# Performance work log

Hardware: AMD Instinct MI355X
Metric: run time of the kernel (lower is better)

## Reference

```python
import jax, jax.numpy as jnp
import numpy as np
from jax import lax

B, A, T, D, V, K = 16, 1024, 512, 256, 50000, 3
EXP_DILS = [1, 2, 4, 8, 16, 32, 32]  # conv_num=7, exp_num=5
REF_DILS = [1, 1, 1]                 # refine_num=3


def setup_inputs() -> dict:
    key = jax.random.key(0)
    ks = jax.random.split(key, 14)
    inp = {
        'article_word': jax.random.randint(ks[0], (B, A), 0, V),
        'article_char': jax.random.randint(ks[1], (B, A, 16), 0, 100),
        'template_word': jax.random.randint(ks[2], (B, T), 0, V),
        'template_char': jax.random.randint(ks[3], (B, T, 16), 0, 100),
        'article_mask': jnp.ones((B, A), jnp.float32),
        'template_mask': jnp.ones((B, T), jnp.float32),
        'emb': jax.random.normal(ks[4], (V, D), jnp.float32) * 0.02,
        'exp_w': jax.random.normal(ks[5], (7, K, D, 2 * D), jnp.float32) * 0.03,
        'exp_b': jnp.zeros((7, 2 * D), jnp.float32),
        'ref_w': jax.random.normal(ks[6], (3, K, D, 2 * D), jnp.float32) * 0.03,
        'ref_b': jnp.zeros((3, 2 * D), jnp.float32),
        'ff1_w': jax.random.normal(ks[7], (10, 10), jnp.float32) * 0.3,
        'ff1_b': jnp.zeros((10,), jnp.float32),
        'ff2_w': jax.random.normal(ks[8], (10, 1), jnp.float32) * 0.3,
        'ff2_b': jnp.zeros((1,), jnp.float32),
    }
    return inp


def _res_block(x, w, b, dilation):
    # x: [B, L, D]; w: [K, D, 2D]  (Conv1d, padding='same' given k//2*dilation)
    pad = (K // 2) * dilation
    y = lax.conv_general_dilated(x, w, window_strides=(1,), padding=[(pad, pad)],
                                 rhs_dilation=(dilation,),
                                 dimension_numbers=('NWC', 'WIO', 'NWC')) + b
    a, g = jnp.split(y, 2, axis=2)  # GLU on channel dim
    return x + a * jax.nn.sigmoid(g)


def _encode(x, exp_w, exp_b, ref_w, ref_b):
    for i, d in enumerate(EXP_DILS):
        x = _res_block(x, exp_w[i], exp_b[i], d)
    for i, d in enumerate(REF_DILS):
        x = _res_block(x, ref_w[i], ref_b[i], d)
    return x  # dropout is identity in eval mode


def reference(article_word, article_char, template_word, template_char,
              article_mask, template_mask, emb, exp_w, exp_b, ref_w, ref_b,
              ff1_w, ff1_b, ff2_w, ff2_b):
    art = _encode(emb[article_word], exp_w, exp_b, ref_w, ref_b)    # [B,A,D]
    tpl = _encode(emb[template_word], exp_w, exp_b, ref_w, ref_b)   # [B,T,D]
    # pairwise squared distance without materializing [B,A,T,D]
    a2 = jnp.sum(art * art, axis=-1)                 # [B,A]
    t2 = jnp.sum(tpl * tpl, axis=-1)                 # [B,T]
    dot = jnp.einsum('bad,btd->bat', art, tpl)       # [B,A,T]
    dist = jnp.maximum(a2[:, :, None] + t2[:, None, :] - 2.0 * dot, 0.0)
    S = jnp.exp(-dist) * article_mask[:, :, None] * template_mask[:, None, :]
    row_max = jnp.max(S, axis=2)                     # [B,A]
    top, _ = lax.top_k(row_max, 10)                  # sorted descending, [B,10]
    h = jax.nn.relu(top @ ff1_w + ff1_b)             # [B,10]
    out = (h @ ff2_w + ff2_b).squeeze()              # [B]
    return out
```

## Files before the change

### kernel.cpp

```cpp
#include <hip/hip_runtime.h>
#include <math.h>

#define NB 16
#define NA 1024
#define NT 512
#define ND 256
#define PAD 32

typedef short bf8_t __attribute__((ext_vector_type(8)));
typedef float f4_t __attribute__((ext_vector_type(4)));

__device__ __forceinline__ float bf2f(ushort u) {
    union { unsigned int i; float f; } v; v.i = ((unsigned int)u) << 16; return v.f;
}
__device__ __forceinline__ ushort f2bf(float f) {
    union { float f; unsigned int i; } v; v.f = f;
    unsigned int x = v.i;
    unsigned int r = (x + 0x7fffu + ((x >> 16) & 1u)) >> 16;
    return (ushort)r;
}
__device__ __forceinline__ void gl_lds16(const void* g, void* l) {
    __builtin_amdgcn_global_load_lds(
        (const __attribute__((address_space(1))) unsigned int*)g,
        (__attribute__((address_space(3))) unsigned int*)l, 16, 0, 0);
}


__global__ void __launch_bounds__(256)
setup_kernel(const int* __restrict__ art_w, const int* __restrict__ tpl_w,
             const float* __restrict__ emb,
             ushort* __restrict__ art_a, ushort* __restrict__ art_b,
             ushort* __restrict__ tpl_a, ushort* __restrict__ tpl_b,
             const float* __restrict__ exp_w, const float* __restrict__ ref_w,
             ushort* __restrict__ wpack,
             float* __restrict__ a2, float* __restrict__ t2) {
    __shared__ float tile[64][65];
    int bid = blockIdx.x;
    int tid = threadIdx.x;

    if (bid < 2048) {
        int idx = bid * 256 + tid;
        int l = idx & (NA - 1);
        int bq = idx >> 10;
        int qq = bq & 31, b = bq >> 5;
        int wd = art_w[b * NA + l];
        const float4* src = (const float4*)(emb + (size_t)wd * ND + qq * 8);
        float4 v0 = src[0], v1 = src[1];
        ushort o[8];
        o[0]=f2bf(v0.x); o[1]=f2bf(v0.y); o[2]=f2bf(v0.z); o[3]=f2bf(v0.w);
        o[4]=f2bf(v1.x); o[5]=f2bf(v1.y); o[6]=f2bf(v1.z); o[7]=f2bf(v1.w);
        *(uint4*)(art_a + ((size_t)bq * (NA + 64) + PAD + l) * 8) = *(uint4*)o;
        return;
    }
    bid -= 2048;
    if (bid < 1024) {
        int j = bid * 256 + tid;
        int l = j & (NT - 1);
        int bq = j >> 9;
        int qq = bq & 31, b = bq >> 5;
        int wd = tpl_w[b * NT + l];
        const float4* src = (const float4*)(emb + (size_t)wd * ND + qq * 8);
        float4 v0 = src[0], v1 = src[1];
        ushort o[8];
        o[0]=f2bf(v0.x); o[1]=f2bf(v0.y); o[2]=f2bf(v0.z); o[3]=f2bf(v0.w);
        o[4]=f2bf(v1.x); o[5]=f2bf(v1.y); o[6]=f2bf(v1.z); o[7]=f2bf(v1.w);
        *(uint4*)(tpl_a + ((size_t)bq * (NT + 64) + PAD + l) * 8) = *(uint4*)o;
        return;
    }
    bid -= 1024;
    if (bid < 512) {
        int j = bid * 256 + tid;
        int y = j >> 15;
        int rem = j & 32767;
        ushort* p = (y == 0) ? art_a : (y == 1) ? art_b : (y == 2) ? tpl_a : tpl_b;
        int L = (y < 2) ? NA : NT;
        int Lp = L + 2 * PAD;
        int plane = rem >> 6;
        int row_in = rem & 63;
        int slab = (row_in < PAD) ? row_in : L + row_in;
        uint4 z = make_uint4(0, 0, 0, 0);
        *(uint4*)(p + ((size_t)plane * Lp + slab) * 8) = z;
        return;
    }
    bid -= 512;
    if (bid < 24) {
        int i = (bid * 256 + tid) * 4;
        float4 z = make_float4(0.f, 0.f, 0.f, 0.f);
        if (i < NB * NA) *(float4*)(a2 + i) = z;
        else             *(float4*)(t2 + i - NB * NA) = z;
        return;
    }
    bid -= 24;
    {
        int li = bid / 96;
        int r = bid % 96;
        int gk = r >> 3;
        int gc = r & 7;
        const float* src = (li < 7) ? exp_w + (size_t)li * 3 * ND * 512
                                    : ref_w + (size_t)(li - 7) * 3 * ND * 512;
        int k0g = gk * 64, c0 = gc * 64;
        #pragma unroll
        for (int p = 0; p < 4; ++p) {
            int kr = p * 16 + (tid >> 4);
            int cc = (tid & 15) * 4;
            *(float4*)&tile[kr][cc] =
                *(const float4*)(src + (size_t)(k0g + kr) * 512 + c0 + cc);
        }
        __syncthreads();
        int tap = k0g >> 8, kl0 = k0g & 255, kc0 = kl0 >> 5;
        int ag = c0 >> 8, cb = (c0 & 255) >> 6;
        int kg = tid >> 5, idx = tid & 31;
        int kc = kc0 + (kg >> 2), qq = kg & 3;
        #pragma unroll
        for (int h = 0; h < 2; ++h) {
            int w64 = idx + h * 32;
            int cprime = h * 64 + ag * 32 + idx;
            ushort o[8];
            #pragma unroll
            for (int j = 0; j < 8; ++j) o[j] = f2bf(tile[kg * 8 + j][w64]);
            ushort* d = wpack +
                (((((size_t)(li * 4 + cb) * 3 + tap) * 8 + kc) * 4 + qq) * 128 + cprime) * 8;
            *(uint4*)d = *(uint4*)o;
        }
    }
}

__global__ void __launch_bounds__(256, 4)
conv_glu_mfma(const ushort* __restrict__ art_x, ushort* __restrict__ art_y,
              const ushort* __restrict__ tpl_x, ushort* __restrict__ tpl_y,
              const ushort* __restrict__ wp, const float* __restrict__ bias,
              int dil, int last, float* __restrict__ a2, float* __restrict__ t2) {
    __shared__ char smem[34816];
    ushort* Abuf = (ushort*)smem;
    float* ylds = (float*)smem;

    const int tid = threadIdx.x;
    const int w = tid >> 6, lane = tid & 63;
    const int wm = w >> 1, wn = w & 1;
    const int q = lane >> 4, l15 = lane & 15;

    const int id = blockIdx.x;
    const int cb = (id >> 3) & 3;
    const int pb = ((id >> 5) << 3) | (id & 7);
    const int plane = pb % 12;
    const int b = pb / 12;
    const int b32 = b * 32;

    int Lp, l0;
    const ushort* xb;
    ushort* yb;
    float* sq;
    int sqbase;
    if (plane < 8) {
        Lp = NA + 2 * PAD; l0 = plane * 128;
        xb = art_x; yb = art_y; sq = a2; sqbase = b * NA + l0;
    } else {
        Lp = NT + 2 * PAD; l0 = (plane - 8) * 128;
        xb = tpl_x; yb = tpl_y; sq = t2; sqbase = b * NT + l0;
    }
    const ushort* wl = wp + (size_t)cb * 98304;
    const int boff = (q * 128 + wn * 64 + l15) * 8;

    f4_t acc[4][4];
    #pragma unroll
    for (int i = 0; i < 4; ++i)
        #pragma unroll
        for (int j = 0; j < 4; ++j)
            acc[i][j] = (f4_t){0.f, 0.f, 0.f, 0.f};

    #pragma unroll
    for (int s3 = 0; s3 < 3; ++s3) {
        int s = w + s3 * 4;
        int qq = s / 3;
        int rphys = l0 + (s % 3) * 64 + lane;
        gl_lds16(xb + ((size_t)(b32 + qq) * Lp + rphys) * 8, Abuf + s * 512);
    }

    for (int kc = 0; kc < 8; ++kc) {
        __syncthreads();
        if (kc < 7) {
            ushort* dst = Abuf + ((kc + 1) & 1) * 6144;
            #pragma unroll
            for (int s3 = 0; s3 < 3; ++s3) {
                int s = w + s3 * 4;
                int qq = (kc + 1) * 4 + s / 3;
                int rphys = l0 + (s % 3) * 64 + lane;
                gl_lds16(xb + ((size_t)(b32 + qq) * Lp + rphys) * 8, dst + s * 512);
            }
        }
        const ushort* Ah = Abuf + (kc & 1) * 6144;
        const ushort* wkc = wl + kc * 4096 + boff;
        #pragma unroll
        for (int t = 0; t < 3; ++t) {
            bf8_t bfr[4];
            #pragma unroll
            for (int nt = 0; nt < 4; ++nt)
                bfr[nt] = *(const bf8_t*)(wkc + t * 32768 + nt * 128);
            const int sh = (t - 1) * dil;
            bf8_t af[4];
            #pragma unroll
            for (int mt = 0; mt < 4; ++mt)
                af[mt] = *(const bf8_t*)(Ah + (q * 192 + 32 + sh + wm * 64 + mt * 16 + l15) * 8);
            #pragma unroll
            for (int mt = 0; mt < 4; ++mt)
                #pragma unroll
                for (int nt = 0; nt < 4; ++nt)
                    acc[mt][nt] = __builtin_amdgcn_mfma_f32_16x16x32_bf16(
                        af[mt], bfr[nt], acc[mt][nt], 0, 0, 0);
        }
    }
    __syncthreads();

    #pragma unroll
    for (int nt = 0; nt < 2; ++nt) {
        const int cl = wn * 32 + nt * 16 + l15;
        const int chan = cb * 64 + cl;
        const float ba = bias[chan];
        const float bg2 = bias[chan + 256];
        #pragma unroll
        for (int mt = 0; mt < 4; ++mt) {
            #pragma unroll
            for (int r = 0; r < 4; ++r) {
                const int row = wm * 64 + mt * 16 + q * 4 + r;
                float av = acc[mt][nt][r] + ba;
                float gv = acc[mt][nt + 2][r] + bg2;
                ylds[row * 68 + cl] = av / (1.f + __expf(-gv));
            }
        }
    }
    __syncthreads();

    float ss = 0.f;
    #pragma unroll
    for (int p = 0; p < 4; ++p) {
        int u = p * 256 + tid;
        int cl8 = u >> 7;
        int row = u & 127;
        size_t go = ((size_t)(b32 + cb * 8 + cl8) * Lp + l0 + PAD + row) * 8;
        ushort xv[8]; *(uint4*)xv = *(const uint4*)(xb + go);
        float4 y0 = *(float4*)&ylds[row * 68 + cl8 * 8];
        float4 y1 = *(float4*)&ylds[row * 68 + cl8 * 8 + 4];
        ushort ov[8];
        ov[0]=f2bf(bf2f(xv[0])+y0.x); ov[1]=f2bf(bf2f(xv[1])+y0.y);
        ov[2]=f2bf(bf2f(xv[2])+y0.z); ov[3]=f2bf(bf2f(xv[3])+y0.w);
        ov[4]=f2bf(bf2f(xv[4])+y1.x); ov[5]=f2bf(bf2f(xv[5])+y1.y);
        ov[6]=f2bf(bf2f(xv[6])+y1.z); ov[7]=f2bf(bf2f(xv[7])+y1.w);
        *(uint4*)(yb + go) = *(uint4*)ov;
        if (last) {
            #pragma unroll
            for (int j = 0; j < 8; ++j) { float f = bf2f(ov[j]); ss += f * f; }
        }
    }
    if (last) {
        float* ssred = (float*)smem;
        __syncthreads();
        ssred[tid] = ss;
        __syncthreads();
        if (tid < 128)
            atomicAdd(&sq[sqbase + tid], ssred[tid] + ssred[tid + 128]);
    }
}

__global__ void __launch_bounds__(256, 4)
dist_rowmax_mfma(const ushort* __restrict__ art, const ushort* __restrict__ tpl,
                 const float* __restrict__ a2, const float* __restrict__ t2,
                 const float* __restrict__ amask, const float* __restrict__ tmask,
                 float* __restrict__ rmaxp) {
    __shared__ ushort Als[2][4 * 512];
    __shared__ ushort Bls[2][8 * 512];
    __shared__ float red[2][64];

    const int tid = threadIdx.x;
    const int w = tid >> 6, lane = tid & 63;
    const int wm = w >> 1, wn = w & 1;
    const int q = lane >> 4, l15 = lane & 15;

    const int id = blockIdx.x;
    const int b = (id & 7) | (((id >> 3) & 1) << 3);
    const int rest = id >> 4;
    const int a0 = (rest & 15) * 64;
    const int tplane = rest >> 4;
    const int t0 = tplane * 128;
    const int b32 = b * 32;
    const int LpA = NA + 2 * PAD, LpT = NT + 2 * PAD;

    float a2v[2][4], amv[2][4];
    #pragma unroll
    for (int mt = 0; mt < 2; ++mt)
        #pragma unroll
        for (int r = 0; r < 4; ++r) {
            int row = a0 + wm * 32 + mt * 16 + q * 4 + r;
            a2v[mt][r] = a2[b * NA + row];
            amv[mt][r] = amask[b * NA + row];
        }

    f4_t acc[2][4];
    #pragma unroll
    for (int i = 0; i < 2; ++i)
        #pragma unroll
        for (int j = 0; j < 4; ++j)
            acc[i][j] = (f4_t){0.f, 0.f, 0.f, 0.f};

    #pragma unroll
    for (int s3 = 0; s3 < 3; ++s3) {
        int s = w + s3 * 4;
        if (s < 4) {
            gl_lds16(art + ((size_t)(b32 + s) * LpA + PAD + a0 + lane) * 8,
                     Als[0] + s * 512);
        } else {
            int s2 = s - 4;
            int qq = s2 >> 1;
            int r0 = (s2 & 1) * 64;
            gl_lds16(tpl + ((size_t)(b32 + qq) * LpT + PAD + t0 + r0 + lane) * 8,
                     Bls[0] + s2 * 512);
        }
    }

    for (int kb = 0; kb < 8; ++kb) {
        __syncthreads();
        if (kb < 7) {
            int nb = (kb + 1) & 1;
            #pragma unroll
            for (int s3 = 0; s3 < 3; ++s3) {
                int s = w + s3 * 4;
                if (s < 4) {
                    int qq = (kb + 1) * 4 + s;
                    gl_lds16(art + ((size_t)(b32 + qq) * LpA + PAD + a0 + lane) * 8,
                             Als[nb] + s * 512);
                } else {
                    int s2 = s - 4;
                    int qq = (kb + 1) * 4 + (s2 >> 1);
                    int r0 = (s2 & 1) * 64;
                    gl_lds16(tpl + ((size_t)(b32 + qq) * LpT + PAD + t0 + r0 + lane) * 8,
                             Bls[nb] + s2 * 512);
                }
            }
        }
        const ushort* Ab = Als[kb & 1];
        const ushort* Bb = Bls[kb & 1];
        bf8_t af[2], bfr[4];
        #pragma unroll
        for (int mt = 0; mt < 2; ++mt)
            af[mt] = *(const bf8_t*)(Ab + (q * 64 + wm * 32 + mt * 16 + l15) * 8);
        #pragma unroll
        for (int nt = 0; nt < 4; ++nt)
            bfr[nt] = *(const bf8_t*)(Bb + (q * 128 + wn * 64 + nt * 16 + l15) * 8);
        #pragma unroll
        for (int mt = 0; mt < 2; ++mt)
            #pragma unroll
            for (int nt = 0; nt < 4; ++nt)
                acc[mt][nt] = __builtin_amdgcn_mfma_f32_16x16x32_bf16(
                    af[mt], bfr[nt], acc[mt][nt], 0, 0, 0);
    }

    float rm[2][4];
    #pragma unroll
    for (int mt = 0; mt < 2; ++mt)
        #pragma unroll
        for (int r = 0; r < 4; ++r) rm[mt][r] = 0.f;

    #pragma unroll
    for (int nt = 0; nt < 4; ++nt) {
        int t = t0 + wn * 64 + nt * 16 + l15;
        float t2v = t2[b * NT + t];
        float tmv = tmask[b * NT + t];
        #pragma unroll
        for (int mt = 0; mt < 2; ++mt)
            #pragma unroll
            for (int r = 0; r < 4; ++r) {
                float d = a2v[mt][r] + t2v - 2.f * acc[mt][nt][r];
                d = fmaxf(d, 0.f);
                float s = __expf(-d) * amv[mt][r] * tmv;
                rm[mt][r] = fmaxf(rm[mt][r], s);
            }
    }
    #pragma unroll
    for (int mt = 0; mt < 2; ++mt)
        #pragma unroll
        for (int r = 0; r < 4; ++r) {
            float v = rm[mt][r];
            #pragma unroll
            for (int off = 1; off < 16; off <<= 1)
                v = fmaxf(v, __shfl_xor(v, off));
            rm[mt][r] = v;
        }
    if (l15 == 0) {
        #pragma unroll
        for (int mt = 0; mt < 2; ++mt)
            #pragma unroll
            for (int r = 0; r < 4; ++r)
                red[wn][wm * 32 + mt * 16 + q * 4 + r] = rm[mt][r];
    }
    __syncthreads();
    if (tid < 64)
        rmaxp[((size_t)tplane * NB + b) * NA + a0 + tid] =
            fmaxf(red[0][tid], red[1][tid]);
}

__global__ void __launch_bounds__(256)
topk_mlp_kernel(const float* __restrict__ rmaxp,
                const float* __restrict__ ff1_w, const float* __restrict__ ff1_b,
                const float* __restrict__ ff2_w, const float* __restrict__ ff2_b,
                float* __restrict__ out) {
    __shared__ float vals[NA];
    __shared__ float top[10];
    __shared__ float h[10];
    __shared__ float rv[4];
    __shared__ int ri[4];

    int b = blockIdx.x;
    int tid = threadIdx.x;
    int lane = tid & 63, wv = tid >> 6;
    for (int i = tid; i < NA; i += 256) {
        float m = rmaxp[(size_t)b * NA + i];
        m = fmaxf(m, rmaxp[((size_t)NB + b) * NA + i]);
        m = fmaxf(m, rmaxp[((size_t)2 * NB + b) * NA + i]);
        m = fmaxf(m, rmaxp[((size_t)3 * NB + b) * NA + i]);
        vals[i] = m;
    }
    __syncthreads();

    for (int it = 0; it < 10; ++it) {
        float best = -1e30f;
        int bi = 0;
        #pragma unroll
        for (int u = 0; u < 4; ++u) {
            int i = u * 256 + tid;
            if (vals[i] > best) { best = vals[i]; bi = i; }
        }
        #pragma unroll
        for (int off = 32; off; off >>= 1) {
            float ob = __shfl_down(best, off);
            int oi = __shfl_down(bi, off);
            if (ob > best) { best = ob; bi = oi; }
        }
        if (lane == 0) { rv[wv] = best; ri[wv] = bi; }
        __syncthreads();
        if (tid == 0) {
            float bb = rv[0]; int bbi = ri[0];
            #pragma unroll
            for (int k = 1; k < 4; ++k)
                if (rv[k] > bb) { bb = rv[k]; bbi = ri[k]; }
            top[it] = bb; vals[bbi] = -1e30f;
        }
        __syncthreads();
    }

    if (tid < 10) {
        float s = ff1_b[tid];
        #pragma unroll
        for (int i = 0; i < 10; ++i) s += top[i] * ff1_w[i * 10 + tid];
        h[tid] = fmaxf(s, 0.f);
    }
    __syncthreads();
    if (tid == 0) {
        float s = ff2_b[0];
        #pragma unroll
        for (int j = 0; j < 10; ++j) s += h[j] * ff2_w[j];
        out[b] = s;
    }
}

extern "C" void kernel_launch(void* const* d_in, const int* in_sizes, int n_in,
                              void* d_out, int out_size, void* d_ws, size_t ws_size,
                              hipStream_t stream) {
    const int*   art_w = (const int*)d_in[0];
    const int*   tpl_w = (const int*)d_in[2];
    const float* amask = (const float*)d_in[4];
    const float* tmask = (const float*)d_in[5];
    const float* emb   = (const float*)d_in[6];
    const float* exp_w = (const float*)d_in[7];
    const float* exp_b = (const float*)d_in[8];
    const float* ref_w = (const float*)d_in[9];
    const float* ref_b = (const float*)d_in[10];
    const float* ff1_w = (const float*)d_in[11];
    const float* ff1_b = (const float*)d_in[12];
    const float* ff2_w = (const float*)d_in[13];
    const float* ff2_b = (const float*)d_in[14];
    float* out = (float*)d_out;

    const size_t art_bytes = (size_t)NB * 32 * (NA + 2 * PAD) * 8 * 2;
    const size_t tpl_bytes = (size_t)NB * 32 * (NT + 2 * PAD) * 8 * 2;
    const size_t wpk_bytes = (size_t)10 * 4 * 3 * 8 * 4 * 128 * 8 * 2;

    char* p = (char*)d_ws;
    ushort* art_a = (ushort*)p; p += art_bytes;
    ushort* art_b = (ushort*)p; p += art_bytes;
    ushort* tpl_a = (ushort*)p; p += tpl_bytes;
    ushort* tpl_b = (ushort*)p; p += tpl_bytes;
    ushort* wpack = (ushort*)p; p += wpk_bytes;
    float* a2    = (float*)p; p += (size_t)NB * NA * 4;
    float* t2    = (float*)p; p += (size_t)NB * NT * 4;
    float* rmaxp = (float*)p; p += (size_t)4 * NB * NA * 4;

    setup_kernel<<<4568, 256, 0, stream>>>(art_w, tpl_w, emb,
                                           art_a, art_b, tpl_a, tpl_b,
                                           exp_w, ref_w, wpack, a2, t2);

    const int dils[10] = {1, 2, 4, 8, 16, 32, 32, 1, 1, 1};

    ushort* a_cur = art_a; ushort* a_nxt = art_b;
    ushort* t_cur = tpl_a; ushort* t_nxt = tpl_b;
    for (int i = 0; i < 10; ++i) {
        const ushort* wl = wpack + (size_t)i * 4 * 98304;
        const float* bb = (i < 7) ? exp_b + (size_t)i * 512
                                  : ref_b + (size_t)(i - 7) * 512;
        conv_glu_mfma<<<768, 256, 0, stream>>>(
            a_cur, a_nxt, t_cur, t_nxt, wl, bb, dils[i], (i == 9) ? 1 : 0, a2, t2);
        ushort* t1 = a_cur; a_cur = a_nxt; a_nxt = t1;
        ushort* t2p = t_cur; t_cur = t_nxt; t_nxt = t2p;
    }
    ushort* art_fin = a_cur;
    ushort* tpl_fin = t_cur;

    dist_rowmax_mfma<<<1024, 256, 0, stream>>>(
        art_fin, tpl_fin, a2, t2, amask, tmask, rmaxp);

    topk_mlp_kernel<<<NB, 256, 0, stream>>>(rmaxp, ff1_w, ff1_b, ff2_w, ff2_b, out);
}
```

Baseline: 404.1 us.

## Replace double-buffered LDS prefetch with single-buffer load-sync-compute loops

Removes the double-buffered global-to-LDS prefetch pipeline in both the conv GLU kernel and the distance kernel, replacing it with a load, barrier, compute, barrier sequence. The conv kernel now loads two K-chunks per stage into the same LDS space, halving the number of stages, while the distance kernel uses single buffers with half the LDS footprint. The aim is simpler synchronization and possibly higher occupancy. The cost is that load latency is no longer hidden behind MFMA work within a block.

```diff
diff --git a/kernel.cpp b/kernel.cpp
--- a/kernel.cpp
+++ b/kernel.cpp
@@ -131,7 +131,7 @@
               const ushort* __restrict__ wp, const float* __restrict__ bias,
               int dil, int last, float* __restrict__ a2, float* __restrict__ t2) {
     __shared__ char smem[34816];
-    ushort* Abuf = (ushort*)smem;
+    ushort* Als = (ushort*)smem;
     float* ylds = (float*)smem;
 
     const int tid = threadIdx.x;
@@ -168,48 +168,43 @@
         for (int j = 0; j < 4; ++j)
             acc[i][j] = (f4_t){0.f, 0.f, 0.f, 0.f};
 
-    #pragma unroll
-    for (int s3 = 0; s3 < 3; ++s3) {
-        int s = w + s3 * 4;
-        int qq = s / 3;
-        int rphys = l0 + (s % 3) * 64 + lane;
-        gl_lds16(xb + ((size_t)(b32 + qq) * Lp + rphys) * 8, Abuf + s * 512);
-    }
-
-    for (int kc = 0; kc < 8; ++kc) {
-        __syncthreads();
-        if (kc < 7) {
-            ushort* dst = Abuf + ((kc + 1) & 1) * 6144;
-            #pragma unroll
-            for (int s3 = 0; s3 < 3; ++s3) {
-                int s = w + s3 * 4;
-                int qq = (kc + 1) * 4 + s / 3;
-                int rphys = l0 + (s % 3) * 64 + lane;
-                gl_lds16(xb + ((size_t)(b32 + qq) * Lp + rphys) * 8, dst + s * 512);
-            }
-        }
-        const ushort* Ah = Abuf + (kc & 1) * 6144;
-        const ushort* wkc = wl + kc * 4096 + boff;
-        #pragma unroll
-        for (int t = 0; t < 3; ++t) {
-            bf8_t bfr[4];
-            #pragma unroll
-            for (int nt = 0; nt < 4; ++nt)
-                bfr[nt] = *(const bf8_t*)(wkc + t * 32768 + nt * 128);
-            const int sh = (t - 1) * dil;
-            bf8_t af[4];
-            #pragma unroll
-            for (int mt = 0; mt < 4; ++mt)
-                af[mt] = *(const bf8_t*)(Ah + (q * 192 + 32 + sh + wm * 64 + mt * 16 + l15) * 8);
-            #pragma unroll
-            for (int mt = 0; mt < 4; ++mt)
+    for (int kc2 = 0; kc2 < 4; ++kc2) {
+        #pragma unroll
+        for (int s3 = 0; s3 < 6; ++s3) {
+            int s = w + s3 * 4;
+            int h = s / 12, within = s % 12;
+            int qq = kc2 * 8 + h * 4 + within / 3;
+            int rphys = l0 + (within % 3) * 64 + lane;
+            gl_lds16(xb + ((size_t)(b32 + qq) * Lp + rphys) * 8, Als + s * 512);
+        }
+        __syncthreads();
+
+        #pragma unroll
+        for (int h = 0; h < 2; ++h) {
+            const int kc = kc2 * 2 + h;
+            const ushort* wkc = wl + kc * 4096 + boff;
+            const ushort* Ah = Als + h * 6144;
+            #pragma unroll
+            for (int t = 0; t < 3; ++t) {
+                bf8_t bfr[4];
                 #pragma unroll
                 for (int nt = 0; nt < 4; ++nt)
-                    acc[mt][nt] = __builtin_amdgcn_mfma_f32_16x16x32_bf16(
-                        af[mt], bfr[nt], acc[mt][nt], 0, 0, 0);
-        }
-    }
-    __syncthreads();
+                    bfr[nt] = *(const bf8_t*)(wkc + t * 32768 + nt * 128);
+                const int sh = (t - 1) * dil;
+                bf8_t af[4];
+                #pragma unroll
+                for (int mt = 0; mt < 4; ++mt)
+                    af[mt] = *(const bf8_t*)(Ah + (q * 192 + 32 + sh + wm * 64 + mt * 16 + l15) * 8);
+                #pragma unroll
+                for (int mt = 0; mt < 4; ++mt)
+                    #pragma unroll
+                    for (int nt = 0; nt < 4; ++nt)
+                        acc[mt][nt] = __builtin_amdgcn_mfma_f32_16x16x32_bf16(
+                            af[mt], bfr[nt], acc[mt][nt], 0, 0, 0);
+            }
+        }
+        __syncthreads();
+    }
 
     #pragma unroll
     for (int nt = 0; nt < 2; ++nt) {
@@ -266,8 +261,8 @@
                  const float* __restrict__ a2, const float* __restrict__ t2,
                  const float* __restrict__ amask, const float* __restrict__ tmask,
                  float* __restrict__ rmaxp) {
-    __shared__ ushort Als[2][4 * 512];
-    __shared__ ushort Bls[2][8 * 512];
+    __shared__ ushort Als[64 * 32];
+    __shared__ ushort Bls[128 * 32];
     __shared__ float red[2][64];
 
     const int tid = threadIdx.x;
@@ -301,56 +296,38 @@
         for (int j = 0; j < 4; ++j)
             acc[i][j] = (f4_t){0.f, 0.f, 0.f, 0.f};
 
-    #pragma unroll
-    for (int s3 = 0; s3 < 3; ++s3) {
-        int s = w + s3 * 4;
-        if (s < 4) {
-            gl_lds16(art + ((size_t)(b32 + s) * LpA + PAD + a0 + lane) * 8,
-                     Als[0] + s * 512);
-        } else {
-            int s2 = s - 4;
-            int qq = s2 >> 1;
-            int r0 = (s2 & 1) * 64;
-            gl_lds16(tpl + ((size_t)(b32 + qq) * LpT + PAD + t0 + r0 + lane) * 8,
-                     Bls[0] + s2 * 512);
-        }
-    }
-
     for (int kb = 0; kb < 8; ++kb) {
-        __syncthreads();
-        if (kb < 7) {
-            int nb = (kb + 1) & 1;
-            #pragma unroll
-            for (int s3 = 0; s3 < 3; ++s3) {
-                int s = w + s3 * 4;
-                if (s < 4) {
-                    int qq = (kb + 1) * 4 + s;
-                    gl_lds16(art + ((size_t)(b32 + qq) * LpA + PAD + a0 + lane) * 8,
-                             Als[nb] + s * 512);
-                } else {
-                    int s2 = s - 4;
-                    int qq = (kb + 1) * 4 + (s2 >> 1);
-                    int r0 = (s2 & 1) * 64;
-                    gl_lds16(tpl + ((size_t)(b32 + qq) * LpT + PAD + t0 + r0 + lane) * 8,
-                             Bls[nb] + s2 * 512);
-                }
+        #pragma unroll
+        for (int s3 = 0; s3 < 3; ++s3) {
+            int s = w + s3 * 4;
+            if (s < 4) {
+                int qq = kb * 4 + s;
+                gl_lds16(art + ((size_t)(b32 + qq) * LpA + PAD + a0 + lane) * 8,
+                         Als + s * 512);
+            } else {
+                int s2 = s - 4;
+                int qq = kb * 4 + (s2 >> 1);
+                int r0 = (s2 & 1) * 64;
+                gl_lds16(tpl + ((size_t)(b32 + qq) * LpT + PAD + t0 + r0 + lane) * 8,
+                         Bls + s2 * 512);
             }
         }
-        const ushort* Ab = Als[kb & 1];
-        const ushort* Bb = Bls[kb & 1];
+        __syncthreads();
+
         bf8_t af[2], bfr[4];
         #pragma unroll
         for (int mt = 0; mt < 2; ++mt)
-            af[mt] = *(const bf8_t*)(Ab + (q * 64 + wm * 32 + mt * 16 + l15) * 8);
+            af[mt] = *(const bf8_t*)(Als + (q * 64 + wm * 32 + mt * 16 + l15) * 8);
         #pragma unroll
         for (int nt = 0; nt < 4; ++nt)
-            bfr[nt] = *(const bf8_t*)(Bb + (q * 128 + wn * 64 + nt * 16 + l15) * 8);
+            bfr[nt] = *(const bf8_t*)(Bls + (q * 128 + wn * 64 + nt * 16 + l15) * 8);
         #pragma unroll
         for (int mt = 0; mt < 2; ++mt)
             #pragma unroll
             for (int nt = 0; nt < 4; ++nt)
                 acc[mt][nt] = __builtin_amdgcn_mfma_f32_16x16x32_bf16(
                     af[mt], bfr[nt], acc[mt][nt], 0, 0, 0);
+        __syncthreads();
     }
 
     float rm[2][4];
```

After: 374.8 us, median of 2. 1.08x faster.
